# Kernel tuning notes

Hardware: AMD Instinct MI355X
Metric: run time of the kernel (lower is better)

The kernel has to match this reference:

```python
import jax, jax.numpy as jnp
import numpy as np
import math

B, S, V, E, D, H, L = 1024, 30, 100000, 300, 512, 8, 4
DK = D // H

def setup_inputs() -> dict:
    key = jax.random.key(0)
    ks = jax.random.split(key, 12)
    sc = 0.02
    return {
        "x": jax.random.randint(ks[0], (B, S), 0, V, dtype=jnp.int32),
        "mask": jax.random.randint(ks[1], (B, 1, 1, S), 0, 2, dtype=jnp.int32),
        "emb": jax.random.normal(ks[2], (V, E), dtype=jnp.float32) * sc,
        "W_in": jax.random.normal(ks[3], (D, E), dtype=jnp.float32) * sc,
        "b_in": jnp.zeros((D,), jnp.float32),
        "Wq": jax.random.normal(ks[4], (L, DK, DK), dtype=jnp.float32) * 0.05,
        "Wk": jax.random.normal(ks[5], (L, DK, DK), dtype=jnp.float32) * 0.05,
        "Wv": jax.random.normal(ks[6], (L, DK, DK), dtype=jnp.float32) * 0.05,
        "Wo": jax.random.normal(ks[7], (L, D, D), dtype=jnp.float32) * sc,
        "Wfc": jax.random.normal(ks[8], (L, D, D), dtype=jnp.float32) * sc,
        "bfc": jnp.zeros((L, D), jnp.float32),
        "g1": jnp.ones((L, D), jnp.float32),
        "beta1": jnp.zeros((L, D), jnp.float32),
        "g2": jnp.ones((L, D), jnp.float32),
        "beta2": jnp.zeros((L, D), jnp.float32),
    }

def _layernorm(x, g, b, eps=1e-5):
    mu = jnp.mean(x, axis=-1, keepdims=True)
    var = jnp.mean(jnp.square(x - mu), axis=-1, keepdims=True)
    return (x - mu) * jax.lax.rsqrt(var + eps) * g + b

def _pos_encoding():
    pos = jnp.arange(S, dtype=jnp.float32)[:, None]
    div = jnp.exp(jnp.arange(0, D, 2, dtype=jnp.float32) * (-math.log(10000.0) / D))
    ang = pos * div  # [S, D/2]
    pe = jnp.zeros((S, D), jnp.float32)
    pe = pe.at[:, 0::2].set(jnp.sin(ang)).at[:, 1::2].set(jnp.cos(ang))
    return pe

def _block(h, mask, Wq, Wk, Wv, Wo, Wfc, bfc, g1, b1, g2, b2):
    xh = h.reshape(B, S, H, DK)
    # per-head shared d_k x d_k projections (nn.Linear: y = x @ W.T)
    q = jnp.einsum('bshk,dk->bhsd', xh, Wq)
    k = jnp.einsum('bshk,dk->bhsd', xh, Wk)
    v = jnp.einsum('bshk,dk->bhsd', xh, Wv)
    scores = jnp.einsum('bhqd,bhkd->bhqk', q, k) / math.sqrt(DK)
    scores = jnp.where(mask == 0, jnp.float32(-1e9), scores)
    p = jax.nn.softmax(scores, axis=-1)
    o = jnp.einsum('bhqk,bhkd->bqhd', p, v).reshape(B, S, D)
    o = o @ Wo.T  # output projection, no bias
    n1 = _layernorm(o + h, g1, b1)
    f = n1 @ Wfc.T + bfc
    return _layernorm(f + n1, g2, b2)

def reference(x, mask, emb, W_in, b_in, Wq, Wk, Wv, Wo, Wfc, bfc, g1, beta1, g2, beta2):
    h = emb[x]                               # [B,S,E] embedding gather
    h = jnp.einsum('bse,de->bsd', h, W_in) + b_in
    h = h * math.sqrt(D) + _pos_encoding()[None]  # positional encoding (dropout=eval no-op)
    for i in range(L):
        h = _block(h, mask, Wq[i], Wk[i], Wv[i], Wo[i], Wfc[i], bfc[i],
                   g1[i], beta1[i], g2[i], beta2[i])
    return h
```

## Files before the change

### kernel.cpp

```cpp
#include <hip/hip_runtime.h>
#include <hip/hip_bf16.h>
#include <math.h>

using bf16 = __hip_bfloat16;
typedef __attribute__((ext_vector_type(8))) short short8;
typedef __attribute__((ext_vector_type(4))) float f32x4;

constexpr int nB = 1024, nS = 30, nE = 300, nD = 512, nH = 8, nL = 4, nDK = 64;
constexpr int nTOK = nB * nS;
constexpr float kSqrtD = 22.627416997969522f;
constexpr float kPEc   = -0.03597789207803244f;

__device__ inline unsigned short bfbits(float f) {
  bf16 h = __float2bfloat16(f);
  return *(unsigned short*)&h;
}
__device__ inline float b2f(short s) {
  return __uint_as_float(((unsigned)(unsigned short)s) << 16);
}
__device__ inline void gload16(const void* g, void* lds) {
  __builtin_amdgcn_global_load_lds(
      (const __attribute__((address_space(1))) unsigned int*)g,
      (__attribute__((address_space(3))) unsigned int*)lds, 16, 0, 0);
}

__global__ __launch_bounds__(256) void cvt_all(
    const float* __restrict__ Wo, const float* __restrict__ Wfc,
    const float* __restrict__ Wq, const float* __restrict__ Wk,
    const float* __restrict__ Wv, const float* __restrict__ Win,
    bf16* __restrict__ wo, bf16* __restrict__ wfc, bf16* __restrict__ wq,
    bf16* __restrict__ wk, bf16* __restrict__ wv, bf16* __restrict__ win,
    float* __restrict__ pe) {
  int i = blockIdx.x * 256 + threadIdx.x;
  if (i < 1048576) {
    wo[i] = __float2bfloat16(Wo[i]);
    wfc[i] = __float2bfloat16(Wfc[i]);
    return;
  }
  i -= 1048576;
  if (i < 16384) {
    wq[i] = __float2bfloat16(Wq[i]);
    wk[i] = __float2bfloat16(Wk[i]);
    wv[i] = __float2bfloat16(Wv[i]);
    return;
  }
  i -= 16384;
  if (i < 163840) {
    int r = i / 320, e = i - r * 320;
    win[i] = __float2bfloat16(e < nE ? Win[r * nE + e] : 0.f);
    return;
  }
  i -= 163840;
  if (i < 15360) {
    int s = i >> 9, d = i & 511;
    float ang = (float)s * expf((float)(d >> 1) * kPEc);
    pe[i] = (d & 1) ? cosf(ang) : sinf(ang);
  }
}

__global__ __launch_bounds__(256) void gather_kernel(const int* __restrict__ x,
                                                     const float* __restrict__ emb,
                                                     bf16* __restrict__ a) {
  int g = blockIdx.x * 256 + threadIdx.x;
  int t = g / 40, ch = g - 40 * t;
  float4 v0 = make_float4(0.f, 0.f, 0.f, 0.f), v1 = v0;
  const float* src = emb + (size_t)x[t] * nE + ch * 8;
  if (ch < 37) { v0 = *(const float4*)src; v1 = *(const float4*)(src + 4); }
  else if (ch == 37) { v0 = *(const float4*)src; }
  ushort4 u0, u1;
  u0.x = bfbits(v0.x); u0.y = bfbits(v0.y); u0.z = bfbits(v0.z); u0.w = bfbits(v0.w);
  u1.x = bfbits(v1.x); u1.y = bfbits(v1.y); u1.z = bfbits(v1.z); u1.w = bfbits(v1.w);
  bf16* dst = a + (size_t)t * 320 + ch * 8;
  *(ushort4*)dst = u0;
  *(ushort4*)(dst + 4) = u1;
}

template <int KA, int EPI, int FIN>
__global__ __launch_bounds__(256, 2) void gemm_fused(
    const bf16* __restrict__ A, const bf16* __restrict__ W,
    const float* __restrict__ bias, const bf16* __restrict__ resid,
    const float* __restrict__ pe, const float* __restrict__ g,
    const float* __restrict__ beta, float* __restrict__ outf,
    bf16* __restrict__ outb) {
  __shared__ __align__(16) char smem[39424];
  bf16* As = (bf16*)smem;
  bf16* Ws = (bf16*)smem + 2048;
  float* tb = (float*)smem;
  float* stats = (float*)(smem + 36864);
  float* stats2 = (float*)(smem + 38912);

  const int tid = threadIdx.x, lane = tid & 63, w = tid >> 6;
  const int q = lane >> 4, c = lane & 15;
  const int m0 = blockIdx.x * 64;

  f32x4 acc[4][8];
#pragma unroll
  for (int i = 0; i < 4; ++i)
#pragma unroll
    for (int j = 0; j < 8; ++j) acc[i][j] = (f32x4){0.f, 0.f, 0.f, 0.f};

  const bf16* Ag = A + (size_t)(m0 + lane) * KA + w * 8;
  const bf16* Wg = W + (size_t)lane * KA + w * 8;
  bf16* AsDst = As + (w * 64) * 8;
  bf16* WsDst = Ws + (w * 512) * 8;

  for (int ks = 0; ks < KA / 32; ++ks) {
    __syncthreads();
    gload16(Ag + ks * 32, AsDst);
#pragma unroll
    for (int j = 0; j < 8; ++j)
      gload16(Wg + (size_t)(j * 64) * KA + ks * 32, WsDst + j * 64 * 8);
    __syncthreads();
    short8 af[4], bfr[8];
#pragma unroll
    for (int mt = 0; mt < 4; ++mt)
      af[mt] = *(const short8*)(As + (q * 64 + mt * 16 + c) * 8);
#pragma unroll
    for (int nt = 0; nt < 8; ++nt)
      bfr[nt] = *(const short8*)(Ws + (q * 512 + w * 128 + nt * 16 + c) * 8);
#pragma unroll
    for (int mt = 0; mt < 4; ++mt)
#pragma unroll
      for (int nt = 0; nt < 8; ++nt)
        acc[mt][nt] = __builtin_amdgcn_mfma_f32_16x16x32_bf16(af[mt], bfr[nt], acc[mt][nt], 0, 0, 0);
  }

  float bias4[8];
#pragma unroll
  for (int nt = 0; nt < 8; ++nt)
    bias4[nt] = bias ? bias[w * 128 + nt * 16 + c] : 0.f;

  if (EPI == 0) {
#pragma unroll
    for (int mt = 0; mt < 4; ++mt)
#pragma unroll
      for (int r = 0; r < 4; ++r) {
        int m = m0 + mt * 16 + q * 4 + r;
        int s = m % nS;
        const float* pes = pe + (size_t)s * nD + w * 128 + c;
#pragma unroll
        for (int nt = 0; nt < 8; ++nt)
          acc[mt][nt][r] = (acc[mt][nt][r] + bias4[nt]) * kSqrtD + pes[nt * 16];
      }
    __syncthreads();
  } else {
    float rs[4][4], rq[4][4];
#pragma unroll
    for (int mt = 0; mt < 4; ++mt)
#pragma unroll
      for (int r = 0; r < 4; ++r) {
        int m = m0 + mt * 16 + q * 4 + r;
        const short* rp = (const short*)(resid + (size_t)m * nD + w * 128 + c);
        float s1 = 0.f, s2 = 0.f;
#pragma unroll
        for (int nt = 0; nt < 8; ++nt) {
          float t = acc[mt][nt][r] + bias4[nt] + b2f(rp[nt * 16]);
          acc[mt][nt][r] = t;
          s1 += t; s2 += t * t;
        }
        rs[mt][r] = s1; rq[mt][r] = s2;
      }
#pragma unroll
    for (int mt = 0; mt < 4; ++mt)
#pragma unroll
      for (int r = 0; r < 4; ++r)
#pragma unroll
        for (int off = 1; off < 16; off <<= 1) {
          rs[mt][r] += __shfl_xor(rs[mt][r], off);
          rq[mt][r] += __shfl_xor(rq[mt][r], off);
        }
#pragma unroll
    for (int mt = 0; mt < 4; ++mt)
#pragma unroll
      for (int r = 0; r < 4; ++r)
        if (c == mt * 4 + r) {
          int row = mt * 16 + q * 4 + r;
          stats[row * 8 + w * 2] = rs[mt][r];
          stats[row * 8 + w * 2 + 1] = rq[mt][r];
        }
    __syncthreads();
    if (tid < 64) {
      float su = 0.f, sq = 0.f;
#pragma unroll
      for (int ww = 0; ww < 4; ++ww) {
        su += stats[tid * 8 + ww * 2];
        sq += stats[tid * 8 + ww * 2 + 1];
      }
      float mu = su * (1.f / nD);
      float var = sq * (1.f / nD) - mu * mu;
      stats2[tid * 2] = mu;
      stats2[tid * 2 + 1] = rsqrtf(var + 1e-5f);
    }
    __syncthreads();
  }

  float* tbw = tb + w * 2048;
  const int l32 = lane & 31, hi = lane >> 5;
  const int colw = w * 128 + l32 * 4;
  float4 g4 = make_float4(0, 0, 0, 0), be4 = g4;
  if (EPI == 1) {
    g4 = *(const float4*)&g[colw];
    be4 = *(const float4*)&beta[colw];
  }
#pragma unroll
  for (int mt = 0; mt < 4; ++mt) {
#pragma unroll
    for (int nt = 0; nt < 8; ++nt)
#pragma unroll
      for (int r = 0; r < 4; ++r)
        tbw[(q * 4 + r) * 128 + nt * 16 + c] = acc[mt][nt][r];
#pragma unroll
    for (int i = 0; i < 8; ++i) {
      float4 v = *(const float4*)&tbw[(i * 64 + lane) * 4];
      int rl = mt * 16 + i * 2 + hi;
      int m = m0 + rl;
      float4 y;
      if (EPI == 1) {
        float mu = stats2[rl * 2], inv = stats2[rl * 2 + 1];
        y.x = (v.x - mu) * inv * g4.x + be4.x;
        y.y = (v.y - mu) * inv * g4.y + be4.y;
        y.z = (v.z - mu) * inv * g4.z + be4.z;
        y.w = (v.w - mu) * inv * g4.w + be4.w;
      } else {
        y = v;
      }
      if (FIN) {
        *(float4*)(outf + (size_t)m * nD + colw) = y;
      } else {
        ushort4 ub;
        ub.x = bfbits(y.x); ub.y = bfbits(y.y); ub.z = bfbits(y.z); ub.w = bfbits(y.w);
        *(ushort4*)(outb + (size_t)m * nD + colw) = ub;
      }
    }
  }
}

__global__ __launch_bounds__(256) void attn_kernel(
    const bf16* __restrict__ wqb, const bf16* __restrict__ wkb,
    const bf16* __restrict__ wvb, const int* __restrict__ mask,
    const bf16* __restrict__ hin, bf16* __restrict__ aout) {
  const int tid = threadIdx.x, lane = tid & 63, w = tid >> 6;
  const int q = lane >> 4, c = lane & 15;
  const int b = blockIdx.x >> 3, hd = blockIdx.x & 7;

  __shared__ __align__(16) bf16 xs[8][32][8];
  __shared__ __align__(16) bf16 wq[8][64][8];
  __shared__ __align__(16) bf16 wk[8][64][8];
  __shared__ __align__(16) bf16 wv[8][64][8];
  __shared__ __align__(16) bf16 qb[8][32][8];
  __shared__ __align__(16) bf16 kb[8][32][8];
  __shared__ __align__(16) bf16 vt[4][64][8];
  __shared__ __align__(16) bf16 pb[4][32][8];
  __shared__ float ps[32][33];
  __shared__ int msk[32];

  {
    int row = tid & 31, k8 = tid >> 5;
    uint4 z = make_uint4(0, 0, 0, 0);
    if (row < nS)
      z = *(const uint4*)(hin + (size_t)(b * nS + row) * nD + hd * nDK + k8 * 8);
    *(uint4*)&xs[k8][row][0] = z;
  }
#pragma unroll
  for (int i = 0; i < 2; ++i) {
    int s = tid + i * 256;
    int row = s & 63, k8 = s >> 6;
    *(uint4*)&wq[k8][row][0] = *(const uint4*)(wqb + row * 64 + k8 * 8);
    *(uint4*)&wk[k8][row][0] = *(const uint4*)(wkb + row * 64 + k8 * 8);
    *(uint4*)&wv[k8][row][0] = *(const uint4*)(wvb + row * 64 + k8 * 8);
  }
  if (tid < nS) msk[tid] = mask[b * nS + tid];
  __syncthreads();

  f32x4 aq[2], ak[2], av[2];
#pragma unroll
  for (int mt = 0; mt < 2; ++mt) {
    aq[mt] = (f32x4){0.f, 0.f, 0.f, 0.f};
    ak[mt] = aq[mt]; av[mt] = aq[mt];
  }
#pragma unroll
  for (int kc = 0; kc < 2; ++kc) {
    short8 xa0 = *(const short8*)&xs[kc * 4 + q][c][0];
    short8 xa1 = *(const short8*)&xs[kc * 4 + q][16 + c][0];
    short8 wqf = *(const short8*)&wq[kc * 4 + q][w * 16 + c][0];
    short8 wkf = *(const short8*)&wk[kc * 4 + q][w * 16 + c][0];
    short8 wvf = *(const short8*)&wv[kc * 4 + q][w * 16 + c][0];
    aq[0] = __builtin_amdgcn_mfma_f32_16x16x32_bf16(xa0, wqf, aq[0], 0, 0, 0);
    aq[1] = __builtin_amdgcn_mfma_f32_16x16x32_bf16(xa1, wqf, aq[1], 0, 0, 0);
    ak[0] = __builtin_amdgcn_mfma_f32_16x16x32_bf16(xa0, wkf, ak[0], 0, 0, 0);
    ak[1] = __builtin_amdgcn_mfma_f32_16x16x32_bf16(xa1, wkf, ak[1], 0, 0, 0);
    av[0] = __builtin_amdgcn_mfma_f32_16x16x32_bf16(xa0, wvf, av[0], 0, 0, 0);
    av[1] = __builtin_amdgcn_mfma_f32_16x16x32_bf16(xa1, wvf, av[1], 0, 0, 0);
  }
  const int dk = w * 16 + c;
#pragma unroll
  for (int mt = 0; mt < 2; ++mt)
#pragma unroll
    for (int r = 0; r < 4; ++r) {
      int i = mt * 16 + q * 4 + r;
      qb[dk >> 3][i][dk & 7] = __float2bfloat16(aq[mt][r]);
      kb[dk >> 3][i][dk & 7] = __float2bfloat16(ak[mt][r]);
      vt[i >> 3][dk][i & 7] = __float2bfloat16(av[mt][r]);
    }
  __syncthreads();

  {
    f32x4 sc = (f32x4){0.f, 0.f, 0.f, 0.f};
    const int is0 = (w >> 1) * 16, js0 = (w & 1) * 16;
#pragma unroll
    for (int kc = 0; kc < 2; ++kc) {
      short8 a = *(const short8*)&qb[kc * 4 + q][is0 + c][0];
      short8 bb = *(const short8*)&kb[kc * 4 + q][js0 + c][0];
      sc = __builtin_amdgcn_mfma_f32_16x16x32_bf16(a, bb, sc, 0, 0, 0);
    }
    int j = js0 + c;
    bool live = (j < nS) && (msk[j] != 0);
#pragma unroll
    for (int r = 0; r < 4; ++r) {
      int i = is0 + q * 4 + r;
      ps[i][j] = live ? sc[r] * 0.125f : -1e9f;
    }
  }
  __syncthreads();

  if (tid < nS * 8) {
    int r = tid >> 3, cc = tid & 7;
    float m = -1e30f;
    for (int j = cc; j < nS; j += 8) m = fmaxf(m, ps[r][j]);
#pragma unroll
    for (int o = 1; o < 8; o <<= 1) m = fmaxf(m, __shfl_xor(m, o));
    float sum = 0.f;
    for (int j = cc; j < nS; j += 8) sum += __expf(ps[r][j] - m);
#pragma unroll
    for (int o = 1; o < 8; o <<= 1) sum += __shfl_xor(sum, o);
    float inv = 1.f / sum;
    for (int j = cc; j < nS; j += 8)
      pb[j >> 3][r][j & 7] = __float2bfloat16(__expf(ps[r][j] - m) * inv);
    if (cc >= 6) pb[3][r][cc] = __float2bfloat16(0.f);
  }
  __syncthreads();

  {
    f32x4 o0 = (f32x4){0.f, 0.f, 0.f, 0.f}, o1 = o0;
    short8 pa0 = *(const short8*)&pb[q][c][0];
    short8 pa1 = *(const short8*)&pb[q][16 + c][0];
    short8 vb = *(const short8*)&vt[q][w * 16 + c][0];
    o0 = __builtin_amdgcn_mfma_f32_16x16x32_bf16(pa0, vb, o0, 0, 0, 0);
    o1 = __builtin_amdgcn_mfma_f32_16x16x32_bf16(pa1, vb, o1, 0, 0, 0);
#pragma unroll
    for (int r = 0; r < 4; ++r) {
      int i0 = q * 4 + r;
      aout[(size_t)(b * nS + i0) * nD + hd * nDK + dk] = __float2bfloat16(o0[r]);
      int i1 = 16 + q * 4 + r;
      if (i1 < nS)
        aout[(size_t)(b * nS + i1) * nD + hd * nDK + dk] = __float2bfloat16(o1[r]);
    }
  }
}

extern "C" void kernel_launch(void* const* d_in, const int* in_sizes, int n_in,
                              void* d_out, int out_size, void* d_ws, size_t ws_size,
                              hipStream_t stream) {
  const int*   x    = (const int*)d_in[0];
  const int*   mask = (const int*)d_in[1];
  const float* emb  = (const float*)d_in[2];
  const float* W_in = (const float*)d_in[3];
  const float* b_in = (const float*)d_in[4];
  const float* Wq   = (const float*)d_in[5];
  const float* Wk   = (const float*)d_in[6];
  const float* Wv   = (const float*)d_in[7];
  const float* Wo   = (const float*)d_in[8];
  const float* Wfc  = (const float*)d_in[9];
  const float* bfc  = (const float*)d_in[10];
  const float* g1   = (const float*)d_in[11];
  const float* be1  = (const float*)d_in[12];
  const float* g2   = (const float*)d_in[13];
  const float* be2  = (const float*)d_in[14];

  char* ws = (char*)d_ws;
  bf16* wo_b  = (bf16*)ws;
  bf16* wfc_b = (bf16*)(ws + 2097152);
  bf16* wq_b  = (bf16*)(ws + 4194304);
  bf16* wk_b  = (bf16*)(ws + 4227072);
  bf16* wv_b  = (bf16*)(ws + 4259840);
  bf16* win_b = (bf16*)(ws + 4292608);
  float* pe   = (float*)(ws + 4620288);
  bf16* a_emb = (bf16*)(ws + 4681728);
  bf16* bufH  = (bf16*)(ws + 24342528);
  bf16* bufO  = (bf16*)(ws + 55799808);
  bf16* bufN  = (bf16*)(ws + 87257088);

  cvt_all<<<4860, 256, 0, stream>>>(Wo, Wfc, Wq, Wk, Wv, W_in, wo_b, wfc_b,
                                    wq_b, wk_b, wv_b, win_b, pe);
  gather_kernel<<<4800, 256, 0, stream>>>(x, emb, a_emb);

  gemm_fused<320, 0, 0><<<480, 256, 0, stream>>>(
      a_emb, win_b, b_in, nullptr, pe, nullptr, nullptr, nullptr, bufH);

  for (int l = 0; l < nL; ++l) {
    attn_kernel<<<nB * nH, 256, 0, stream>>>(
        wq_b + l * 4096, wk_b + l * 4096, wv_b + l * 4096, mask, bufH, bufO);
    gemm_fused<512, 1, 0><<<480, 256, 0, stream>>>(
        bufO, wo_b + (size_t)l * 262144, nullptr, bufH, nullptr, g1 + l * nD,
        be1 + l * nD, nullptr, bufN);
    if (l < nL - 1) {
      gemm_fused<512, 1, 0><<<480, 256, 0, stream>>>(
          bufN, wfc_b + (size_t)l * 262144, bfc + l * nD, bufN, nullptr,
          g2 + l * nD, be2 + l * nD, nullptr, bufH);
    } else {
      gemm_fused<512, 1, 1><<<480, 256, 0, stream>>>(
          bufN, wfc_b + (size_t)l * 262144, bfc + l * nD, bufN, nullptr,
          g2 + l * nD, be2 + l * nD, (float*)d_out, nullptr);
    }
  }
  (void)in_sizes; (void)n_in; (void)out_size; (void)ws_size;
}
```

Measured before the change: 637.1 us.

## Double-buffer GEMM LDS tiles to overlap global loads with MFMA compute

Splits LDS into two buffers and issues the async global-to-LDS loads for the next K slice before computing the current one. Explicit vmcnt waits and barriers replace the paired __syncthreads. The goal is to hide global load latency behind the MFMA work. It roughly doubles shared memory per block to about 76 KB, which may reduce how many blocks fit per CU under the launch bound of 2. It also relies on the hand-written vmcnt count matching the number of loads in flight.

```diff
diff --git a/kernel.cpp b/kernel.cpp
--- a/kernel.cpp
+++ b/kernel.cpp
@@ -82,16 +82,15 @@
     const float* __restrict__ pe, const float* __restrict__ g,
     const float* __restrict__ beta, float* __restrict__ outf,
     bf16* __restrict__ outb) {
-  __shared__ __align__(16) char smem[39424];
-  bf16* As = (bf16*)smem;
-  bf16* Ws = (bf16*)smem + 2048;
+  __shared__ __align__(16) char smem[76288];
   float* tb = (float*)smem;
-  float* stats = (float*)(smem + 36864);
-  float* stats2 = (float*)(smem + 38912);
+  float* stats = (float*)(smem + 73728);
+  float* stats2 = (float*)(smem + 75776);
 
   const int tid = threadIdx.x, lane = tid & 63, w = tid >> 6;
   const int q = lane >> 4, c = lane & 15;
   const int m0 = blockIdx.x * 64;
+  constexpr int NK = KA / 32;
 
   f32x4 acc[4][8];
 #pragma unroll
@@ -101,16 +100,29 @@
 
   const bf16* Ag = A + (size_t)(m0 + lane) * KA + w * 8;
   const bf16* Wg = W + (size_t)lane * KA + w * 8;
-  bf16* AsDst = As + (w * 64) * 8;
-  bf16* WsDst = Ws + (w * 512) * 8;
-
-  for (int ks = 0; ks < KA / 32; ++ks) {
-    __syncthreads();
-    gload16(Ag + ks * 32, AsDst);
+
+  auto stage = [&](int ks, int buf) {
+    bf16* Asb = (bf16*)(smem + buf * 36864);
+    bf16* Wsb = Asb + 2048;
+    gload16(Ag + ks * 32, Asb + (w * 64) * 8);
 #pragma unroll
     for (int j = 0; j < 8; ++j)
-      gload16(Wg + (size_t)(j * 64) * KA + ks * 32, WsDst + j * 64 * 8);
-    __syncthreads();
+      gload16(Wg + (size_t)(j * 64) * KA + ks * 32, Wsb + ((size_t)(w * 512 + j * 64)) * 8);
+  };
+
+  stage(0, 0);
+  for (int ks = 0; ks < NK; ++ks) {
+    const int cur = ks & 1;
+    if (ks + 1 < NK) {
+      stage(ks + 1, cur ^ 1);
+      asm volatile("s_waitcnt vmcnt(9)" ::: "memory");
+    } else {
+      asm volatile("s_waitcnt vmcnt(0)" ::: "memory");
+    }
+    __builtin_amdgcn_s_barrier();
+    asm volatile("" ::: "memory");
+    const bf16* As = (const bf16*)(smem + cur * 36864);
+    const bf16* Ws = As + 2048;
     short8 af[4], bfr[8];
 #pragma unroll
     for (int mt = 0; mt < 4; ++mt)
@@ -123,6 +135,9 @@
 #pragma unroll
       for (int nt = 0; nt < 8; ++nt)
         acc[mt][nt] = __builtin_amdgcn_mfma_f32_16x16x32_bf16(af[mt], bfr[nt], acc[mt][nt], 0, 0, 0);
+    asm volatile("" ::: "memory");
+    __builtin_amdgcn_s_barrier();
+    asm volatile("" ::: "memory");
   }
 
   float bias4[8];
```

After: 642.3 us. Within noise of the previous version (+0.8%).
